# Kernel tuning notes

Measured on AMD Instinct MI355X. Metric: run time of the kernel, lower is better.

## Reference

```python
import jax, jax.numpy as jnp
import numpy as np

D_MODEL = 256      # num_nodes == d_model (forced by pre_relation mask shape)
MW = 2             # moving_window (hardcoded '2' in MPNN reshape)
STRIDE = 1
DECAY = 0.7
INPUT_DIM = 64
OUTPUT_DIM = 64
BN_EPS = 1e-5


def _mask_matrix():
    # Mask_Matrix: block (i,j) of size d_model x d_model equals decay**|i-j|
    blocks = DECAY ** np.abs(np.arange(MW)[:, None] - np.arange(MW)[None, :])
    return jnp.asarray(np.kron(blocks, np.ones((D_MODEL, D_MODEL))).astype(np.float32))


def _bn(h, w, b):
    # training-mode BatchNorm1d over channel-last layout [B, N, C]
    mu = h.mean(axis=(0, 1))
    var = h.var(axis=(0, 1))  # biased variance, as torch uses for normalization
    return (h - mu) * jax.lax.rsqrt(var + BN_EPS) * w + b


def setup_inputs() -> dict:
    key = jax.random.key(0)
    ks = jax.random.split(key, 4)
    bs, scale_num = 16, 17
    x = jax.random.normal(ks[0], (bs, scale_num, D_MODEL, INPUT_DIM), jnp.float32)
    # mapping2 weights scaled small to keep the dot-product softmax well conditioned
    w_map2 = jax.random.normal(ks[1], (INPUT_DIM, INPUT_DIM), jnp.float32) * 0.05
    b_map2 = jnp.zeros((INPUT_DIM,), jnp.float32)
    bn0_w = jnp.ones((INPUT_DIM,), jnp.float32)
    bn0_b = jnp.zeros((INPUT_DIM,), jnp.float32)
    th0_w = jax.random.normal(ks[2], (OUTPUT_DIM, INPUT_DIM), jnp.float32) / np.float32(np.sqrt(INPUT_DIM))
    th0_b = jnp.zeros((OUTPUT_DIM,), jnp.float32)
    th1_w = jax.random.normal(ks[3], (OUTPUT_DIM, INPUT_DIM), jnp.float32) / np.float32(np.sqrt(INPUT_DIM))
    th1_b = jnp.zeros((OUTPUT_DIM,), jnp.float32)
    bn1_w = jnp.ones((OUTPUT_DIM,), jnp.float32)
    bn1_b = jnp.zeros((OUTPUT_DIM,), jnp.float32)
    return dict(x=x, w_map2=w_map2, b_map2=b_map2, bn0_w=bn0_w, bn0_b=bn0_b,
                th0_w=th0_w, th0_b=th0_b, th1_w=th1_w, th1_b=th1_b,
                bn1_w=bn1_w, bn1_b=bn1_b)


def reference(x, w_map2, b_map2, bn0_w, bn0_b, th0_w, th0_b, th1_w, th1_b, bn1_w, bn1_b):
    bs, S, N, F = x.shape
    L = (S - MW) // STRIDE + 1  # num_windows from F.unfold
    # WindowConv_Graph + transpose(2,3) + reshape: X[b,l,m,n,f] = x[b, l*stride+m, n, f]
    idx = np.arange(L)[:, None] * STRIDE + np.arange(MW)[None, :]
    X = x[:, idx].reshape(bs * L, MW * N, F)  # [B', N1, F]

    # Dot_Graph_Construction_weights (N1 != d_model -> mapping2 branch)
    nf = X @ w_map2.T + b_map2                       # [B', N1, F]
    adj = jnp.einsum('bnf,bmf->bnm', nf, nf)         # [B', N1, N1]
    eye = jnp.eye(MW * N, dtype=x.dtype)
    adj = jax.nn.leaky_relu(adj - eye * 1e8)
    adj = jax.nn.softmax(adj, axis=-1) + eye

    # decay mask multiply
    adj = adj * _mask_matrix()

    # BatchNorm over input_dim channels
    xb = _bn(nf, bn0_w, bn0_b)

    # MPNN_mk_v2, field=2, way='sum'
    out = (adj @ xb) @ th0_w.T + th0_b               # hop 1
    adj2 = adj @ adj
    out = out + (adj2 @ xb) @ th1_w.T + th1_b        # hop 2
    out = jax.nn.leaky_relu(_bn(out, bn1_w, bn1_b))

    # pooling over the moving_window axis (mean), then over windows (mean)
    out = out.reshape(bs, L, MW, N, OUTPUT_DIM).mean(axis=2)
    return out.mean(axis=1)  # [bs, num_nodes, output_dim]
```

## Files before the change

kernel.cpp:

```cpp
#include <hip/hip_runtime.h>


typedef unsigned short u16;
typedef __bf16 bf16x8 __attribute__((ext_vector_type(8)));
typedef float f32x4 __attribute__((ext_vector_type(4)));
typedef unsigned int u32x4 __attribute__((ext_vector_type(4)));

#define MFMA16(a, b, c) __builtin_amdgcn_mfma_f32_16x16x32_bf16(a, b, c, 0, 0, 0)

#define BSZ 16
#define SNUM 17
#define FD 64
#define NB 256
#define N1 512
#define SL_ELEMS 16384
#define Y_ELEMS (BSZ * SNUM * SL_ELEMS)

#define WM_O 0
#define BM_O 4096
#define B0W_O 4160
#define B0B_O 4224
#define T0W_O 4288
#define T0B_O 8384
#define T1W_O 8448
#define T1B_O 12544
#define B1W_O 12608
#define B1B_O 12672
#define P_TOT 12736

#define SLAB2_O 32768
#define RED_O 65536
#define SCR_O 65792
#define LDS_U16 (SCR_O + 16 * 640)

__device__ __forceinline__ float bf2f(u16 u) {
    union { unsigned int i; float f; } v;
    v.i = ((unsigned int)u) << 16;
    return v.f;
}
__device__ __forceinline__ u16 f2bu(float f) {
    __bf16 h = (__bf16)f;
    return __builtin_bit_cast(u16, h);
}
__device__ __forceinline__ u16 f2bf(float f) {
    unsigned int u = __builtin_bit_cast(unsigned int, f);
    unsigned int r = (u + 0x7fffu + ((u >> 16) & 1u)) >> 16;
    return (u16)r;
}
__device__ __forceinline__ bf16x8 ld8g(const u16* p) {
    return __builtin_bit_cast(bf16x8, *reinterpret_cast<const u32x4*>(p));
}

__global__ __launch_bounds__(256) void k_prep(
    const void* p0, const void* p1, const void* p2, const void* p3,
    const void* p4, const void* p5, const void* p6, const void* p7,
    const void* p8, const void* p9, int* __restrict__ flagOut,
    u16* __restrict__ pc, float* __restrict__ stats) {
    const int tid = threadIdx.x, lane = tid & 63;
    int z = 0, bc = 0;
    const unsigned int* w = (const unsigned int*)p0;
    for (int i = lane; i < 2048; i += 64) {
        const unsigned int v = w[i];
        z += ((v & 0xffffu) == 0u);
        bc += (v >> 14) & 1;
    }
#pragma unroll
    for (int o = 1; o < 64; o <<= 1) {
        z += __shfl_xor(z, o);
        bc += __shfl_xor(bc, o);
    }
    const int flag = (z > 1024 || bc > 256) ? 1 : 0;
    if (blockIdx.x == 0) {
        if (tid == 0) *flagOut = flag;
        if (tid < 256) stats[tid] = 0.f;
    }
    const int i = blockIdx.x * 256 + tid;
    if (i >= P_TOT) return;
    const void* src;
    int si;
    if (i < BM_O)        { src = p0; si = i; }
    else if (i < B0W_O)  { src = p1; si = i - BM_O; }
    else if (i < B0B_O)  { src = p2; si = i - B0W_O; }
    else if (i < T0W_O)  { src = p3; si = i - B0B_O; }
    else if (i < T0B_O)  { src = p4; si = i - T0W_O; }
    else if (i < T1W_O)  { src = p5; si = i - T0B_O; }
    else if (i < T1B_O)  { src = p6; si = i - T1W_O; }
    else if (i < B1W_O)  { src = p7; si = i - T1B_O; }
    else if (i < B1B_O)  { src = p8; si = i - B1W_O; }
    else                 { src = p9; si = i - B1B_O; }
    pc[i] = flag ? f2bf(((const float*)src)[si]) : ((const u16*)src)[si];
}

__global__ __launch_bounds__(256) void k_y(const void* __restrict__ xv,
                                           const int* __restrict__ flag,
                                           const u16* __restrict__ pc,
                                           u16* __restrict__ y,
                                           float* __restrict__ gstats) {
    const int slice = blockIdx.x;
    const int tid = threadIdx.x, wave = tid >> 6, lane = tid & 63;
    const int quad = lane >> 4, l16 = lane & 15;
    __shared__ float red[128];
    if (tid < 128) red[tid] = 0.f;
    const int isf32 = *flag;

    f32x4 acc[4][4];
#pragma unroll
    for (int i = 0; i < 4; i++)
#pragma unroll
        for (int j = 0; j < 4; j++) acc[i][j] = (f32x4){0.f, 0.f, 0.f, 0.f};

    bf16x8 bfr[4][2];
#pragma unroll
    for (int nt = 0; nt < 4; nt++)
#pragma unroll
        for (int kh = 0; kh < 2; kh++)
            bfr[nt][kh] = ld8g(pc + WM_O + (nt * 16 + l16) * 64 + kh * 32 + quad * 8);

    const float* xf = (const float*)xv + (size_t)slice * SL_ELEMS;
    const u16* xh = (const u16*)xv + (size_t)slice * SL_ELEMS;

#pragma unroll
    for (int mt = 0; mt < 4; mt++) {
        const int row = wave * 64 + mt * 16 + l16;
        bf16x8 a0, a1;
        if (isf32) {
            const float* r0 = xf + row * 64 + quad * 8;
            f32x4 v0 = *(const f32x4*)r0;
            f32x4 v1 = *(const f32x4*)(r0 + 4);
            f32x4 v2 = *(const f32x4*)(r0 + 32);
            f32x4 v3 = *(const f32x4*)(r0 + 36);
#pragma unroll
            for (int j = 0; j < 4; j++) {
                a0[j] = (__bf16)v0[j]; a0[4 + j] = (__bf16)v1[j];
                a1[j] = (__bf16)v2[j]; a1[4 + j] = (__bf16)v3[j];
            }
        } else {
            a0 = ld8g(xh + row * 64 + quad * 8);
            a1 = ld8g(xh + row * 64 + 32 + quad * 8);
        }
#pragma unroll
        for (int nt = 0; nt < 4; nt++)
            acc[mt][nt] = MFMA16(a1, bfr[nt][1], MFMA16(a0, bfr[nt][0], acc[mt][nt]));
    }

    u16* ys = y + (size_t)slice * SL_ELEMS;
    float s1[4] = {0.f, 0.f, 0.f, 0.f}, s2[4] = {0.f, 0.f, 0.f, 0.f};
#pragma unroll
    for (int nt = 0; nt < 4; nt++) {
        const int col = nt * 16 + l16;
        const float bias = bf2f(pc[BM_O + col]);
#pragma unroll
        for (int mt = 0; mt < 4; mt++)
#pragma unroll
            for (int r = 0; r < 4; r++) {
                const int row = wave * 64 + mt * 16 + quad * 4 + r;
                const float v = acc[mt][nt][r] + bias;
                ys[row * 64 + col] = f2bu(v);
                s1[nt] += v;
                s2[nt] += v * v;
            }
        s1[nt] += __shfl_xor(s1[nt], 16); s1[nt] += __shfl_xor(s1[nt], 32);
        s2[nt] += __shfl_xor(s2[nt], 16); s2[nt] += __shfl_xor(s2[nt], 32);
    }
    __syncthreads();
    if (quad == 0) {
#pragma unroll
        for (int nt = 0; nt < 4; nt++) {
            atomicAdd(&red[nt * 16 + l16], s1[nt]);
            atomicAdd(&red[64 + nt * 16 + l16], s2[nt]);
        }
    }
    __syncthreads();
    const int s = slice % SNUM;
    const float wgt = (s == 0 || s == SNUM - 1) ? 1.f : 2.f;
    if (tid < 128) atomicAdd(&gstats[tid], red[tid] * wgt);
}

__device__ __forceinline__ void stage_slab1(u16* slab1, const u16* ybase,
                                            int tid) {
#pragma unroll
    for (int i = 0; i < 4; i++) {
        const int gid = i * 1024 + tid, n = gid >> 3, g = gid & 7;
        *(u32x4*)(slab1 + n * 64 + ((g ^ (n & 7)) << 3)) =
            *(const u32x4*)(ybase + n * 64 + g * 8);
    }
}

__global__ __launch_bounds__(1024)
__attribute__((amdgpu_waves_per_eu(4, 4)))
void k_h1(const u16* __restrict__ y, const float* __restrict__ stats,
          const u16* __restrict__ pc, u16* __restrict__ z1img) {
    __shared__ u16 lds[LDS_U16];
    u16* slab1 = lds;
    u16* slab2 = lds + SLAB2_O;
    const int tid = threadIdx.x, w = tid >> 6, lane = tid & 63;
    const int quad = lane >> 4, l16 = lane & 15;
    u16* scr = lds + SCR_O + w * 640;
    const int g = blockIdx.x, p = g >> 1, half = g & 1;
    const int b = p >> 4, l = p & 15;
    const f32x4 ZERO4 = (f32x4){0.f, 0.f, 0.f, 0.f};

    const float cinv = 1.f / 131072.f;
    const int fme = tid & 63;
    float mu0 = stats[fme] * cinv;
    float vr0 = fmaxf(stats[64 + fme] * cinv - mu0 * mu0, 0.f);
    const float scale_f = rsqrtf(vr0 + 1e-5f) * bf2f(pc[B0W_O + fme]);
    const float shift_f = bf2f(pc[B0B_O + fme]) - mu0 * scale_f;

    const u16* ybase = y + (size_t)(b * SNUM + l) * SL_ELEMS;
    stage_slab1(slab1, ybase, tid);
    __syncthreads();

#pragma unroll
    for (int i = 0; i < 4; i++) {
        const int gn = (tid >> 6) + i * 16;
        union { u16 u[8]; u32x4 v; } pk;
#pragma unroll
        for (int j = 0; j < 8; j++) {
            const int n = gn * 8 + j;
            const u16 raw = slab1[n * 64 + (((fme >> 3) ^ (n & 7)) << 3) + (fme & 7)];
            pk.u[j] = f2bu(bf2f(raw) * scale_f + shift_f);
        }
        *(u32x4*)(slab2 + fme * 512 + ((gn ^ fme) << 3)) = pk.v;
    }
    __syncthreads();

    const int rowbase = half * 256 + w * 16;
    bf16x8 a[2];
#pragma unroll
    for (int h = 0; h < 2; h++) {
        const int row = rowbase + l16;
        a[h] = *(const bf16x8*)(slab1 + row * 64 + (((h * 4 + quad) ^ (row & 7)) << 3));
    }

    const float mb = (half == 0) ? 0.7f : (1.0f / 0.7f);
    const float me = (half == 0) ? (1.0f / 0.7f) : 1.0f;

    f32x4 oacc[4];
    f32x4 lsum = ZERO4;
#pragma unroll
    for (int ft = 0; ft < 4; ft++) oacc[ft] = ZERO4;

#pragma unroll 1
    for (int c = 0; c < 8; c++) {
        if (c == 4) {
#pragma unroll
            for (int r = 0; r < 4; r++) lsum[r] *= mb;
        }
        const float lmf = ((half == 1) == (c >= 4)) ? 0.f : -0.5145731728f;
#pragma unroll
        for (int ch = 0; ch < 2; ch++) {
            const int colbase = c * 64 + ch * 32;
            f32x4 S[2];
#pragma unroll
            for (int jt = 0; jt < 2; jt++) {
                const int rj = colbase + jt * 16 + l16;
                const bf16x8 b0 = *(const bf16x8*)(slab1 + rj * 64 + ((quad ^ (rj & 7)) << 3));
                const bf16x8 b1 = *(const bf16x8*)(slab1 + rj * 64 + (((4 + quad) ^ (rj & 7)) << 3));
                S[jt] = MFMA16(a[1], b1, MFMA16(a[0], b0, ZERO4));
            }
#pragma unroll
            for (int jt = 0; jt < 2; jt++)
#pragma unroll
                for (int r = 0; r < 4; r++) {
                    const float s = S[jt][r];
                    const float m2 = s > 0.f ? 1.44269504f : 0.0144269504f;
                    float pv = exp2f(fminf(fmaf(s, m2, lmf), 86.f));
                    if (colbase + jt * 16 == rowbase && l16 == quad * 4 + r) pv = 0.f;
                    lsum[r] += pv;
                    scr[(quad * 4 + r) * 40 + jt * 16 + l16] = f2bu(pv);
                }
            const bf16x8 pa = *(const bf16x8*)(scr + l16 * 40 + quad * 8);
#pragma unroll
            for (int ft = 0; ft < 4; ft++) {
                const int f = ft * 16 + l16, gn = c * 8 + ch * 4 + quad;
                const bf16x8 bv = *(const bf16x8*)(slab2 + f * 512 + ((gn ^ f) << 3));
                oacc[ft] = MFMA16(pa, bv, oacc[ft]);
            }
        }
    }
#pragma unroll
    for (int r = 0; r < 4; r++) {
        lsum[r] += __shfl_xor(lsum[r], 1);
        lsum[r] += __shfl_xor(lsum[r], 2);
        lsum[r] += __shfl_xor(lsum[r], 4);
        lsum[r] += __shfl_xor(lsum[r], 8);
    }

    f32x4 inv;
#pragma unroll
    for (int r = 0; r < 4; r++) inv[r] = __builtin_amdgcn_rcpf(lsum[r] * me);
#pragma unroll
    for (int ft = 0; ft < 4; ft++)
#pragma unroll
        for (int r = 0; r < 4; r++) {
            const int i = rowbase + quad * 4 + r;
            const int f = ft * 16 + l16;
            const float xbv = bf2f(slab2[f * 512 + (((i >> 3) ^ f) << 3) + (i & 7)]);
            oacc[ft][r] = oacc[ft][r] * inv[r] + xbv;
        }
    __syncthreads();
#pragma unroll
    for (int ft = 0; ft < 4; ft++)
#pragma unroll
        for (int r = 0; r < 4; r++) {
            const int i = rowbase + quad * 4 + r;
            const int f = ft * 16 + l16;
            slab2[f * 512 + (((i >> 3) ^ f) << 3) + (i & 7)] = f2bu(oacc[ft][r]);
        }
    __syncthreads();
    {
        const int fr = tid >> 4, seg = tid & 15;
        const int off = (((half * 32) ^ (fr & 32)) << 3) + seg * 16;
        u16* dst = z1img + (size_t)p * 32768 + fr * 512 + off;
        const u16* srcp = slab2 + fr * 512 + off;
        *(u32x4*)(dst) = *(const u32x4*)(srcp);
        *(u32x4*)(dst + 8) = *(const u32x4*)(srcp + 8);
    }
}

__global__ __launch_bounds__(1024)
__attribute__((amdgpu_waves_per_eu(4, 4)))
void k_h2(const u16* __restrict__ y, const u16* __restrict__ z1img,
          float* __restrict__ stats, const u16* __restrict__ pc,
          u16* __restrict__ opre) {
    __shared__ u16 lds[LDS_U16];
    u16* slab1 = lds;
    u16* slab2 = lds + SLAB2_O;
    float* red = (float*)(lds + RED_O);
    const int tid = threadIdx.x, w = tid >> 6, lane = tid & 63;
    const int quad = lane >> 4, l16 = lane & 15;
    u16* scr = lds + SCR_O + w * 640;
    const int g = blockIdx.x, p = g >> 1, half = g & 1;
    const int b = p >> 4, l = p & 15;
    const f32x4 ZERO4 = (f32x4){0.f, 0.f, 0.f, 0.f};

    if (tid < 128) red[tid] = 0.f;

    const u16* ybase = y + (size_t)(b * SNUM + l) * SL_ELEMS;
    stage_slab1(slab1, ybase, tid);

    const u16* zsrc = z1img + (size_t)p * 32768;
#pragma unroll
    for (int i = 0; i < 4; i++) {
        const int gid = i * 1024 + tid;
        *(u32x4*)(slab2 + gid * 8) = *(const u32x4*)(zsrc + gid * 8);
    }
    __syncthreads();

    const int rowbase = half * 256 + w * 16;
    bf16x8 a[2];
#pragma unroll
    for (int h = 0; h < 2; h++) {
        const int row = rowbase + l16;
        a[h] = *(const bf16x8*)(slab1 + row * 64 + (((h * 4 + quad) ^ (row & 7)) << 3));
    }

    const float mb = (half == 0) ? 0.7f : (1.0f / 0.7f);
    const float me = (half == 0) ? (1.0f / 0.7f) : 1.0f;

    f32x4 oacc[4];
    f32x4 lsum = ZERO4;
#pragma unroll
    for (int ft = 0; ft < 4; ft++) oacc[ft] = ZERO4;

#pragma unroll 1
    for (int c = 0; c < 8; c++) {
        if (c == 4) {
#pragma unroll
            for (int r = 0; r < 4; r++) lsum[r] *= mb;
        }
        const float lmf = ((half == 1) == (c >= 4)) ? 0.f : -0.5145731728f;
#pragma unroll
        for (int ch = 0; ch < 2; ch++) {
            const int colbase = c * 64 + ch * 32;
            f32x4 S[2];
#pragma unroll
            for (int jt = 0; jt < 2; jt++) {
                const int rj = colbase + jt * 16 + l16;
                const bf16x8 b0 = *(const bf16x8*)(slab1 + rj * 64 + ((quad ^ (rj & 7)) << 3));
                const bf16x8 b1 = *(const bf16x8*)(slab1 + rj * 64 + (((4 + quad) ^ (rj & 7)) << 3));
                S[jt] = MFMA16(a[1], b1, MFMA16(a[0], b0, ZERO4));
            }
#pragma unroll
            for (int jt = 0; jt < 2; jt++)
#pragma unroll
                for (int r = 0; r < 4; r++) {
                    const float s = S[jt][r];
                    const float m2 = s > 0.f ? 1.44269504f : 0.0144269504f;
                    float pv = exp2f(fminf(fmaf(s, m2, lmf), 86.f));
                    if (colbase + jt * 16 == rowbase && l16 == quad * 4 + r) pv = 0.f;
                    lsum[r] += pv;
                    scr[(quad * 4 + r) * 40 + jt * 16 + l16] = f2bu(pv);
                }
            const bf16x8 pa = *(const bf16x8*)(scr + l16 * 40 + quad * 8);
#pragma unroll
            for (int ft = 0; ft < 4; ft++) {
                const int f = ft * 16 + l16, gn = c * 8 + ch * 4 + quad;
                const bf16x8 bv = *(const bf16x8*)(slab2 + f * 512 + ((gn ^ f) << 3));
                oacc[ft] = MFMA16(pa, bv, oacc[ft]);
            }
        }
    }
#pragma unroll
    for (int r = 0; r < 4; r++) {
        lsum[r] += __shfl_xor(lsum[r], 1);
        lsum[r] += __shfl_xor(lsum[r], 2);
        lsum[r] += __shfl_xor(lsum[r], 4);
        lsum[r] += __shfl_xor(lsum[r], 8);
    }

    float s1a[4] = {0.f, 0.f, 0.f, 0.f}, s2a[4] = {0.f, 0.f, 0.f, 0.f};
    f32x4 inv;
#pragma unroll
    for (int r = 0; r < 4; r++) inv[r] = __builtin_amdgcn_rcpf(lsum[r] * me);
#pragma unroll
    for (int ft = 0; ft < 4; ft++)
#pragma unroll
        for (int r = 0; r < 4; r++) {
            const int i = rowbase + quad * 4 + r;
            const int f = ft * 16 + l16;
            const float o1 = bf2f(slab2[f * 512 + (((i >> 3) ^ f) << 3) + (i & 7)]);
            oacc[ft][r] = oacc[ft][r] * inv[r] + o1;
        }
    bf16x8 a1[2], a2[2];
    const int irow = rowbase + l16;
#pragma unroll
    for (int h = 0; h < 2; h++)
#pragma unroll
        for (int j = 0; j < 8; j++) {
            const int f = h * 32 + quad * 8 + j;
            const u16 raw = slab2[f * 512 + (((irow >> 3) ^ f) << 3) + (irow & 7)];
            a1[h][j] = __builtin_bit_cast(__bf16, raw);
        }
#pragma unroll
    for (int h = 0; h < 2; h++) {
#pragma unroll
        for (int ftl = 0; ftl < 2; ftl++)
#pragma unroll
            for (int r = 0; r < 4; r++)
                scr[(quad * 4 + r) * 40 + ftl * 16 + l16] = f2bu(oacc[2 * h + ftl][r]);
        a2[h] = *(const bf16x8*)(scr + l16 * 40 + quad * 8);
    }
    f32x4 pacc[4];
#pragma unroll
    for (int ot = 0; ot < 4; ot++) {
        const int o = ot * 16 + l16;
        const float bias = bf2f(pc[T0B_O + o]) + bf2f(pc[T1B_O + o]);
        pacc[ot] = (f32x4){bias, bias, bias, bias};
    }
#pragma unroll
    for (int h = 0; h < 2; h++)
#pragma unroll
        for (int ot = 0; ot < 4; ot++) {
            const int o = ot * 16 + l16;
            bf16x8 w0f = ld8g(pc + T0W_O + o * 64 + h * 32 + quad * 8);
            bf16x8 w1f = ld8g(pc + T1W_O + o * 64 + h * 32 + quad * 8);
            pacc[ot] = MFMA16(a1[h], w0f, pacc[ot]);
            pacc[ot] = MFMA16(a2[h], w1f, pacc[ot]);
        }
#pragma unroll
    for (int ot = 0; ot < 4; ot++)
#pragma unroll
        for (int r = 0; r < 4; r++) {
            const int i = rowbase + quad * 4 + r;
            const int o = ot * 16 + l16;
            const float v = pacc[ot][r];
            s1a[ot] += v;
            s2a[ot] += v * v;
            opre[(size_t)p * (N1 * FD) + (size_t)i * 64 + o] = f2bu(v);
        }
#pragma unroll
    for (int ot = 0; ot < 4; ot++) {
        s1a[ot] += __shfl_xor(s1a[ot], 16); s1a[ot] += __shfl_xor(s1a[ot], 32);
        s2a[ot] += __shfl_xor(s2a[ot], 16); s2a[ot] += __shfl_xor(s2a[ot], 32);
    }
    if (quad == 0) {
#pragma unroll
        for (int ot = 0; ot < 4; ot++) {
            atomicAdd(&red[ot * 16 + l16], s1a[ot]);
            atomicAdd(&red[64 + ot * 16 + l16], s2a[ot]);
        }
    }
    __syncthreads();
    if (tid < 128) atomicAdd(&stats[128 + tid], red[tid]);
}

__global__ __launch_bounds__(256) void k_final(const u16* __restrict__ op,
                                               const float* __restrict__ stats,
                                               const u16* __restrict__ pc,
                                               float* __restrict__ out) {
    const int o = blockIdx.x * 256 + threadIdx.x;
    const int f = o & 63, n = (o >> 6) & 255, b = o >> 14;
    const float inv = 1.f / 131072.f;
    const float mu = stats[128 + f] * inv;
    const float var = fmaxf(stats[192 + f] * inv - mu * mu, 0.f);
    const float rs = rsqrtf(var + 1e-5f);
    const float scale = rs * bf2f(pc[B1W_O + f]);
    const float shift = bf2f(pc[B1B_O + f]) - mu * scale;
    float acc = 0.f;
    for (int l = 0; l < 16; l++) {
        const size_t pb = (size_t)(b * 16 + l) * N1 * FD;
#pragma unroll
        for (int m = 0; m < 2; m++) {
            float v = bf2f(op[pb + (size_t)(m * 256 + n) * 64 + f]);
            v = v * scale + shift;
            acc += (v > 0.f ? v : 0.01f * v);
        }
    }
    out[o] = acc * (1.f / 32.f);
}

extern "C" void kernel_launch(void* const* d_in, const int* in_sizes, int n_in,
                              void* d_out, int out_size, void* d_ws, size_t ws_size,
                              hipStream_t stream) {
    char* ws = (char*)d_ws;
    size_t off = 0;
    auto alloc = [&](size_t bytes) { void* pp = ws + off; off += (bytes + 255) & ~(size_t)255; return pp; };
    u16* y = (u16*)alloc((size_t)Y_ELEMS * 2);
    u16* z1img = (u16*)alloc((size_t)NB * 32768 * 2);
    u16* opre = (u16*)alloc((size_t)NB * N1 * FD * 2);
    u16* pc = (u16*)alloc(P_TOT * 2);
    float* stats = (float*)alloc(256 * 4);
    int* flag = (int*)alloc(256);
    float* out = (float*)d_out;

    k_prep<<<50, 256, 0, stream>>>(d_in[1], d_in[2], d_in[3], d_in[4], d_in[5],
                                   d_in[6], d_in[7], d_in[8], d_in[9], d_in[10],
                                   flag, pc, stats);
    k_y<<<BSZ * SNUM, 256, 0, stream>>>(d_in[0], flag, pc, y, stats);
    k_h1<<<2 * NB, 1024, 0, stream>>>(y, stats, pc, z1img);
    k_h2<<<2 * NB, 1024, 0, stream>>>(y, z1img, stats, pc, opre);
    k_final<<<1024, 256, 0, stream>>>(opre, stats, pc, out);
}
```

Measured before the change: 210.2 us.

## Compute transposed score tiles so softmax probabilities feed MFMA directly from registers

The score MFMA now runs with swapped operands and a permuted column mapping, so each lane's accumulator outputs already form the bf16x8 A-operand for the P·V MFMA. This removes the per-wave LDS scratch round-trip for probabilities. It also changes the row-sum reduction to one scalar per lane with cross-quad shuffles plus a broadcast shuffle. A new swizzle function keeps bank-conflict-free LDS reads under the new row access pattern.

```diff
diff --git a/kernel.cpp b/kernel.cpp
--- a/kernel.cpp
+++ b/kernel.cpp
@@ -49,6 +49,9 @@
 }
 __device__ __forceinline__ bf16x8 ld8g(const u16* p) {
     return __builtin_bit_cast(bf16x8, *reinterpret_cast<const u32x4*>(p));
+}
+__device__ __forceinline__ int fsw(int n) {
+    return (n & 3) | ((n >> 1) & 4);
 }
 
 __global__ __launch_bounds__(256) void k_prep(
@@ -181,7 +184,7 @@
 #pragma unroll
     for (int i = 0; i < 4; i++) {
         const int gid = i * 1024 + tid, n = gid >> 3, g = gid & 7;
-        *(u32x4*)(slab1 + n * 64 + ((g ^ (n & 7)) << 3)) =
+        *(u32x4*)(slab1 + n * 64 + ((g ^ fsw(n)) << 3)) =
             *(const u32x4*)(ybase + n * 64 + g * 8);
     }
 }
@@ -195,7 +198,6 @@
     u16* slab2 = lds + SLAB2_O;
     const int tid = threadIdx.x, w = tid >> 6, lane = tid & 63;
     const int quad = lane >> 4, l16 = lane & 15;
-    u16* scr = lds + SCR_O + w * 640;
     const int g = blockIdx.x, p = g >> 1, half = g & 1;
     const int b = p >> 4, l = p & 15;
     const f32x4 ZERO4 = (f32x4){0.f, 0.f, 0.f, 0.f};
@@ -218,7 +220,7 @@
 #pragma unroll
         for (int j = 0; j < 8; j++) {
             const int n = gn * 8 + j;
-            const u16 raw = slab1[n * 64 + (((fme >> 3) ^ (n & 7)) << 3) + (fme & 7)];
+            const u16 raw = slab1[n * 64 + (((fme >> 3) ^ fsw(n)) << 3) + (fme & 7)];
             pk.u[j] = f2bu(bf2f(raw) * scale_f + shift_f);
         }
         *(u32x4*)(slab2 + fme * 512 + ((gn ^ fme) << 3)) = pk.v;
@@ -230,47 +232,45 @@
 #pragma unroll
     for (int h = 0; h < 2; h++) {
         const int row = rowbase + l16;
-        a[h] = *(const bf16x8*)(slab1 + row * 64 + (((h * 4 + quad) ^ (row & 7)) << 3));
+        a[h] = *(const bf16x8*)(slab1 + row * 64 + (((h * 4 + quad) ^ fsw(row)) << 3));
     }
 
     const float mb = (half == 0) ? 0.7f : (1.0f / 0.7f);
     const float me = (half == 0) ? (1.0f / 0.7f) : 1.0f;
 
     f32x4 oacc[4];
-    f32x4 lsum = ZERO4;
+    float lsum = 0.f;
 #pragma unroll
     for (int ft = 0; ft < 4; ft++) oacc[ft] = ZERO4;
 
 #pragma unroll 1
     for (int c = 0; c < 8; c++) {
-        if (c == 4) {
-#pragma unroll
-            for (int r = 0; r < 4; r++) lsum[r] *= mb;
-        }
+        if (c == 4) lsum *= mb;
         const float lmf = ((half == 1) == (c >= 4)) ? 0.f : -0.5145731728f;
 #pragma unroll
         for (int ch = 0; ch < 2; ch++) {
             const int colbase = c * 64 + ch * 32;
             f32x4 S[2];
 #pragma unroll
-            for (int jt = 0; jt < 2; jt++) {
-                const int rj = colbase + jt * 16 + l16;
-                const bf16x8 b0 = *(const bf16x8*)(slab1 + rj * 64 + ((quad ^ (rj & 7)) << 3));
-                const bf16x8 b1 = *(const bf16x8*)(slab1 + rj * 64 + (((4 + quad) ^ (rj & 7)) << 3));
-                S[jt] = MFMA16(a[1], b1, MFMA16(a[0], b0, ZERO4));
+            for (int m = 0; m < 2; m++) {
+                const int rj = colbase + (l16 & 3) + ((l16 >> 2) << 3) + m * 4;
+                const bf16x8 b0 = *(const bf16x8*)(slab1 + rj * 64 + ((quad ^ fsw(rj)) << 3));
+                const bf16x8 b1 = *(const bf16x8*)(slab1 + rj * 64 + (((4 + quad) ^ fsw(rj)) << 3));
+                S[m] = MFMA16(b1, a[1], MFMA16(b0, a[0], ZERO4));
             }
-#pragma unroll
-            for (int jt = 0; jt < 2; jt++)
+            union { u16 u[8]; bf16x8 v; } pkp;
+#pragma unroll
+            for (int m = 0; m < 2; m++)
 #pragma unroll
                 for (int r = 0; r < 4; r++) {
-                    const float s = S[jt][r];
+                    const float s = S[m][r];
                     const float m2 = s > 0.f ? 1.44269504f : 0.0144269504f;
                     float pv = exp2f(fminf(fmaf(s, m2, lmf), 86.f));
-                    if (colbase + jt * 16 == rowbase && l16 == quad * 4 + r) pv = 0.f;
-                    lsum[r] += pv;
-                    scr[(quad * 4 + r) * 40 + jt * 16 + l16] = f2bu(pv);
+                    if (colbase + quad * 8 + m * 4 + r == rowbase + l16) pv = 0.f;
+                    lsum += pv;
+                    pkp.u[m * 4 + r] = f2bu(pv);
                 }
-            const bf16x8 pa = *(const bf16x8*)(scr + l16 * 40 + quad * 8);
+            const bf16x8 pa = pkp.v;
 #pragma unroll
             for (int ft = 0; ft < 4; ft++) {
                 const int f = ft * 16 + l16, gn = c * 8 + ch * 4 + quad;
@@ -279,17 +279,13 @@
             }
         }
     }
-#pragma unroll
-    for (int r = 0; r < 4; r++) {
-        lsum[r] += __shfl_xor(lsum[r], 1);
-        lsum[r] += __shfl_xor(lsum[r], 2);
-        lsum[r] += __shfl_xor(lsum[r], 4);
-        lsum[r] += __shfl_xor(lsum[r], 8);
-    }
-
+    lsum += __shfl_xor(lsum, 16);
+    lsum += __shfl_xor(lsum, 32);
     f32x4 inv;
 #pragma unroll
-    for (int r = 0; r < 4; r++) inv[r] = __builtin_amdgcn_rcpf(lsum[r] * me);
+    for (int r = 0; r < 4; r++)
+        inv[r] = __builtin_amdgcn_rcpf(__shfl(lsum, quad * 4 + r) * me);
+
 #pragma unroll
     for (int ft = 0; ft < 4; ft++)
 #pragma unroll
@@ -353,47 +349,45 @@
 #pragma unroll
     for (int h = 0; h < 2; h++) {
         const int row = rowbase + l16;
-        a[h] = *(const bf16x8*)(slab1 + row * 64 + (((h * 4 + quad) ^ (row & 7)) << 3));
+        a[h] = *(const bf16x8*)(slab1 + row * 64 + (((h * 4 + quad) ^ fsw(row)) << 3));
     }
 
     const float mb = (half == 0) ? 0.7f : (1.0f / 0.7f);
     const float me = (half == 0) ? (1.0f / 0.7f) : 1.0f;
 
     f32x4 oacc[4];
-    f32x4 lsum = ZERO4;
+    float lsum = 0.f;
 #pragma unroll
     for (int ft = 0; ft < 4; ft++) oacc[ft] = ZERO4;
 
 #pragma unroll 1
     for (int c = 0; c < 8; c++) {
-        if (c == 4) {
-#pragma unroll
-            for (int r = 0; r < 4; r++) lsum[r] *= mb;
-        }
+        if (c == 4) lsum *= mb;
         const float lmf = ((half == 1) == (c >= 4)) ? 0.f : -0.5145731728f;
 #pragma unroll
         for (int ch = 0; ch < 2; ch++) {
             const int colbase = c * 64 + ch * 32;
             f32x4 S[2];
 #pragma unroll
-            for (int jt = 0; jt < 2; jt++) {
-                const int rj = colbase + jt * 16 + l16;
-                const bf16x8 b0 = *(const bf16x8*)(slab1 + rj * 64 + ((quad ^ (rj & 7)) << 3));
-                const bf16x8 b1 = *(const bf16x8*)(slab1 + rj * 64 + (((4 + quad) ^ (rj & 7)) << 3));
-                S[jt] = MFMA16(a[1], b1, MFMA16(a[0], b0, ZERO4));
+            for (int m = 0; m < 2; m++) {
+                const int rj = colbase + (l16 & 3) + ((l16 >> 2) << 3) + m * 4;
+                const bf16x8 b0 = *(const bf16x8*)(slab1 + rj * 64 + ((quad ^ fsw(rj)) << 3));
+                const bf16x8 b1 = *(const bf16x8*)(slab1 + rj * 64 + (((4 + quad) ^ fsw(rj)) << 3));
+                S[m] = MFMA16(b1, a[1], MFMA16(b0, a[0], ZERO4));
             }
-#pragma unroll
-            for (int jt = 0; jt < 2; jt++)
+            union { u16 u[8]; bf16x8 v; } pkp;
+#pragma unroll
+            for (int m = 0; m < 2; m++)
 #pragma unroll
                 for (int r = 0; r < 4; r++) {
-                    const float s = S[jt][r];
+                    const float s = S[m][r];
                     const float m2 = s > 0.f ? 1.44269504f : 0.0144269504f;
                     float pv = exp2f(fminf(fmaf(s, m2, lmf), 86.f));
-                    if (colbase + jt * 16 == rowbase && l16 == quad * 4 + r) pv = 0.f;
-                    lsum[r] += pv;
-                    scr[(quad * 4 + r) * 40 + jt * 16 + l16] = f2bu(pv);
+                    if (colbase + quad * 8 + m * 4 + r == rowbase + l16) pv = 0.f;
+                    lsum += pv;
+                    pkp.u[m * 4 + r] = f2bu(pv);
                 }
-            const bf16x8 pa = *(const bf16x8*)(scr + l16 * 40 + quad * 8);
+            const bf16x8 pa = pkp.v;
 #pragma unroll
             for (int ft = 0; ft < 4; ft++) {
                 const int f = ft * 16 + l16, gn = c * 8 + ch * 4 + quad;
@@ -402,18 +396,14 @@
             }
         }
     }
-#pragma unroll
-    for (int r = 0; r < 4; r++) {
-        lsum[r] += __shfl_xor(lsum[r], 1);
-        lsum[r] += __shfl_xor(lsum[r], 2);
-        lsum[r] += __shfl_xor(lsum[r], 4);
-        lsum[r] += __shfl_xor(lsum[r], 8);
-    }
+    lsum += __shfl_xor(lsum, 16);
+    lsum += __shfl_xor(lsum, 32);
+    f32x4 inv;
+#pragma unroll
+    for (int r = 0; r < 4; r++)
+        inv[r] = __builtin_amdgcn_rcpf(__shfl(lsum, quad * 4 + r) * me);
 
     float s1a[4] = {0.f, 0.f, 0.f, 0.f}, s2a[4] = {0.f, 0.f, 0.f, 0.f};
-    f32x4 inv;
-#pragma unroll
-    for (int r = 0; r < 4; r++) inv[r] = __builtin_amdgcn_rcpf(lsum[r] * me);
 #pragma unroll
     for (int ft = 0; ft < 4; ft++)
 #pragma unroll
```

After: 201.5 us. 1.04x faster.
